# Optimization experiments

Measured on AMD Instinct MI355X. Metric: run time of the kernel, lower is better.

The kernel has to match this reference:

```python
import jax, jax.numpy as jnp
import numpy as np

HIDDEN = 1024
HEADS = 16
HEAD_DIM = HIDDEN // HEADS  # 64
LOCAL = (128, 128)
ROPE_MAX_POS = LOCAL[0] + LOCAL[1]  # 256 (local attention branch)
ROPE_BASE = 10000.0


def make_rope_cache(max_len, dim, base):
    positions = jnp.arange(max_len, dtype=jnp.float32)
    theta = 1.0 / base ** (jnp.arange(0, dim, 2, dtype=jnp.float32) / dim)
    angles = jnp.einsum('i,j->ij', positions, theta)
    return jnp.stack([jnp.cos(angles), jnp.sin(angles)], axis=-1)  # (max_len, dim//2, 2)


def apply_rope(x, cache):
    # x: (B, S, H, D); cache: (max_pos, D//2, 2)
    S = x.shape[1]
    pos = jnp.arange(S) % cache.shape[0]
    rc = cache[pos][None, :, None, :, :]  # (1, S, 1, D//2, 2)
    xr = x.reshape(*x.shape[:-1], -1, 2)
    x0, x1 = xr[..., 0], xr[..., 1]
    c, s = rc[..., 0], rc[..., 1]
    out = jnp.stack([x0 * c - x1 * s, x1 * c + x0 * s], axis=-1)
    return out.reshape(x.shape)


def sliding_window_mask(S, window, dtype):
    rel = jnp.arange(S)[:, None] - jnp.arange(S)[None, :]
    inside = (rel >= -window[0]) & (rel <= window[1])
    return jnp.where(inside, jnp.zeros((), dtype), -jnp.inf)[None, None]  # (1,1,S,S)


def setup_inputs() -> dict:
    key = jax.random.key(0)
    k1, k2, k3, k4, k5 = jax.random.split(key, 5)
    B, S = 2, 2048
    hidden_states = jax.random.normal(k1, (B, S, HIDDEN), dtype=jnp.float32)
    Wqkv_kernel = jax.random.normal(k2, (HIDDEN, 3 * HIDDEN), dtype=jnp.float32) / np.sqrt(HIDDEN)
    Wqkv_bias = jnp.zeros((3 * HIDDEN,), dtype=jnp.float32)
    Wo_kernel = jax.random.normal(k3, (HIDDEN, HIDDEN), dtype=jnp.float32) / np.sqrt(HIDDEN)
    Wo_bias = jnp.zeros((HIDDEN,), dtype=jnp.float32)
    rope_cache = make_rope_cache(ROPE_MAX_POS, HEAD_DIM, ROPE_BASE)
    return {
        'hidden_states': hidden_states,
        'Wqkv_kernel': Wqkv_kernel,
        'Wqkv_bias': Wqkv_bias,
        'Wo_kernel': Wo_kernel,
        'Wo_bias': Wo_bias,
        'rope_cache': rope_cache,
    }


def reference(hidden_states, Wqkv_kernel, Wqkv_bias, Wo_kernel, Wo_bias, rope_cache):
    B, S, _ = hidden_states.shape
    qkv = hidden_states @ Wqkv_kernel + Wqkv_bias  # (B,S,3*HIDDEN)
    qkv = qkv.reshape(B, S, 3, HEADS, HEAD_DIM)
    q = qkv[:, :, 0]  # (B,S,H,D)
    k = qkv[:, :, 1]
    v = qkv[:, :, 2]
    q = apply_rope(q, rope_cache)
    k = apply_rope(k, rope_cache)
    # to (B,H,S,D)
    q = jnp.transpose(q, (0, 2, 1, 3))
    k = jnp.transpose(k, (0, 2, 1, 3))
    v = jnp.transpose(v, (0, 2, 1, 3))
    scale = jnp.sqrt(jnp.float32(HEAD_DIM))
    scores = jnp.einsum('bhqd,bhkd->bhqk', q, k) / scale
    mask = sliding_window_mask(S, LOCAL, scores.dtype)
    probs = jax.nn.softmax(scores + mask, axis=-1)
    out = jnp.einsum('bhqk,bhkd->bqhd', probs, v).reshape(B, S, HIDDEN)
    out = out @ Wo_kernel + Wo_bias
    return out
```

## Files before the change

### kernel.cpp

```cpp
#include <hip/hip_runtime.h>
#include <hip/hip_bf16.h>

typedef __bf16 bf16x8 __attribute__((ext_vector_type(8)));
typedef __bf16 bf16x4 __attribute__((ext_vector_type(4)));
typedef float f32x4 __attribute__((ext_vector_type(4)));

#define SLEN 2048
#define NHEADS 16
#define HDIM 64

__global__ __launch_bounds__(256) void prep(const float* __restrict__ hidden,
                                            const float* __restrict__ Wqkv,
                                            const float* __restrict__ Wo,
                                            __bf16* __restrict__ A1,
                                            __bf16* __restrict__ Wt,
                                            __bf16* __restrict__ Wot) {
    int b = blockIdx.x;
    if (b < 4096) {
        int i = b * 256 + threadIdx.x;
        float4 v = reinterpret_cast<const float4*>(hidden)[i];
        bf16x4 o = { (__bf16)v.x, (__bf16)v.y, (__bf16)v.z, (__bf16)v.w };
        reinterpret_cast<bf16x4*>(A1)[i] = o;
    } else {
        __shared__ float tile[32][33];
        const float* W; __bf16* Dst; int N, bx, by;
        if (b < 7168) { int bb = b - 4096; W = Wqkv; Dst = Wt;  N = 3072; bx = bb % 96; by = bb / 96; }
        else          { int bb = b - 7168; W = Wo;   Dst = Wot; N = 1024; bx = bb % 32; by = bb / 32; }
        int tx = threadIdx.x & 31, ty = threadIdx.x >> 5;
        int n0 = bx * 32, k0 = by * 32;
        #pragma unroll
        for (int i = ty; i < 32; i += 8)
            tile[i][tx] = W[(size_t)(k0 + i) * N + n0 + tx];
        __syncthreads();
        #pragma unroll
        for (int i = ty; i < 32; i += 8)
            Dst[(size_t)(n0 + i) * 1024 + k0 + tx] = (__bf16)tile[tx][i];
    }
}

template <int TN>
__global__ __launch_bounds__(256) void gemm_bt(const __bf16* __restrict__ A,
                                               const __bf16* __restrict__ Bt,
                                               const float* __restrict__ bias,
                                               float* __restrict__ Cf,
                                               __bf16* __restrict__ Cq,
                                               __bf16* __restrict__ Ck,
                                               __bf16* __restrict__ Cv,
                                               int M, int N, int K, int epi) {
    constexpr int JN = TN / 32;
    __shared__ __align__(16) __bf16 As[128 * 40];
    __shared__ __align__(16) __bf16 Bs[TN * 40];

    int nb = N / TN;
    int bx = blockIdx.x % nb;
    int by = blockIdx.x / nb;
    int row0 = by * 128, col0 = bx * TN;

    int tid = threadIdx.x;
    int wave = tid >> 6, lane = tid & 63;
    int quad = lane >> 4, lrow = lane & 15;
    int wm = wave >> 1, wn = wave & 1;

    int r1 = tid >> 2;
    int kk = (tid & 3) * 8;
    const __bf16* Aptr = A + (size_t)(row0 + r1) * K + kk;
    const __bf16* Bptr = Bt + (size_t)(col0 + r1) * K + kk;

    f32x4 acc[4][JN];
    f32x4 zero = {0.f, 0.f, 0.f, 0.f};
    #pragma unroll
    for (int i = 0; i < 4; i++)
        #pragma unroll
        for (int j = 0; j < JN; j++) acc[i][j] = zero;

    for (int k0 = 0; k0 < K; k0 += 32) {
        bf16x8 a0 = *reinterpret_cast<const bf16x8*>(Aptr + k0);
        bf16x8 a1 = *reinterpret_cast<const bf16x8*>(Aptr + (size_t)64 * K + k0);
        bf16x8 b0 = *reinterpret_cast<const bf16x8*>(Bptr + k0);
        bf16x8 b1;
        if (TN == 128) b1 = *reinterpret_cast<const bf16x8*>(Bptr + (size_t)64 * K + k0);
        __syncthreads();
        *reinterpret_cast<bf16x8*>(&As[r1 * 40 + kk]) = a0;
        *reinterpret_cast<bf16x8*>(&As[(r1 + 64) * 40 + kk]) = a1;
        *reinterpret_cast<bf16x8*>(&Bs[r1 * 40 + kk]) = b0;
        if (TN == 128) *reinterpret_cast<bf16x8*>(&Bs[(r1 + 64) * 40 + kk]) = b1;
        __syncthreads();

        bf16x8 af[4], bfr[JN];
        #pragma unroll
        for (int i = 0; i < 4; i++)
            af[i] = *reinterpret_cast<const bf16x8*>(&As[(wm * 64 + i * 16 + lrow) * 40 + quad * 8]);
        #pragma unroll
        for (int j = 0; j < JN; j++)
            bfr[j] = *reinterpret_cast<const bf16x8*>(&Bs[(wn * (TN / 2) + j * 16 + lrow) * 40 + quad * 8]);
        #pragma unroll
        for (int i = 0; i < 4; i++)
            #pragma unroll
            for (int j = 0; j < JN; j++)
                acc[i][j] = __builtin_amdgcn_mfma_f32_16x16x32_bf16(af[i], bfr[j], acc[i][j], 0, 0, 0);
    }

    int part = col0 >> 10;
    #pragma unroll
    for (int i = 0; i < 4; i++) {
        int rowb = row0 + wm * 64 + i * 16 + quad * 4;
        #pragma unroll
        for (int j = 0; j < JN; j++) {
            int col = col0 + wn * (TN / 2) + j * 16 + lrow;
            float bsv = bias[col];
            #pragma unroll
            for (int r = 0; r < 4; r++) {
                int row = rowb + r;
                float v = acc[i][j][r] + bsv;
                if (epi == 0) {
                    Cf[(size_t)row * N + col] = v;
                } else {
                    int h = (col >> 6) & 15;
                    int d = col & 63;
                    int b = row >> 11;
                    int s = row & 2047;
                    __bf16* dst = (part == 0) ? Cq : ((part == 1) ? Ck : Cv);
                    dst[((size_t)(b * NHEADS + h) * SLEN + s) * HDIM + d] = (__bf16)v;
                }
            }
        }
    }
}

__device__ __forceinline__ bf16x8 rope8(bf16x8 v, f32x4 a, f32x4 b) {
    bf16x8 o;
    float e, od;
    e = (float)v[0]; od = (float)v[1];
    o[0] = (__bf16)(e * a[0] - od * a[1]); o[1] = (__bf16)(od * a[0] + e * a[1]);
    e = (float)v[2]; od = (float)v[3];
    o[2] = (__bf16)(e * a[2] - od * a[3]); o[3] = (__bf16)(od * a[2] + e * a[3]);
    e = (float)v[4]; od = (float)v[5];
    o[4] = (__bf16)(e * b[0] - od * b[1]); o[5] = (__bf16)(od * b[0] + e * b[1]);
    e = (float)v[6]; od = (float)v[7];
    o[6] = (__bf16)(e * b[2] - od * b[3]); o[7] = (__bf16)(od * b[2] + e * b[3]);
    return o;
}

__global__ __launch_bounds__(256) void attn_kernel(const __bf16* __restrict__ Q,
                                                   const __bf16* __restrict__ K,
                                                   const __bf16* __restrict__ V,
                                                   const float* __restrict__ rope,
                                                   __bf16* __restrict__ O) {
    __shared__ __align__(16) __bf16 Vt[64][328];
    __shared__ __align__(16) __bf16 Pl[4][16][40];

    int qt = blockIdx.x & 31;
    int bh = blockIdx.x >> 5;
    int q0 = qt * 64;
    int kbase0 = q0 - 128;
    const __bf16* Qbh = Q + (size_t)bh * SLEN * HDIM;
    const __bf16* Kbh = K + (size_t)bh * SLEN * HDIM;
    const __bf16* Vbh = V + (size_t)bh * SLEN * HDIM;

    int tid = threadIdx.x;
    int wave = tid >> 6, lane = tid & 63;
    int quad = lane >> 4, lrow = lane & 15;
    int wq0 = q0 + wave * 16;

    {
        int dchunk = wave * 16;
        #pragma unroll
        for (int k = 0; k < 5; k++) {
            int off = k * 64 + lane;
            int krow = kbase0 + off;
            krow = min(max(krow, 0), SLEN - 1);
            const __bf16* vp = Vbh + (size_t)krow * HDIM + dchunk;
            bf16x8 v0 = *reinterpret_cast<const bf16x8*>(vp);
            bf16x8 v1 = *reinterpret_cast<const bf16x8*>(vp + 8);
            #pragma unroll
            for (int i = 0; i < 8; i++) {
                Vt[dchunk + i][off] = v0[i];
                Vt[dchunk + 8 + i][off] = v1[i];
            }
        }
    }

    int posq = (wq0 + lrow) & 255;
    const float* rq = rope + (size_t)posq * 64;
    f32x4 qc0a = *reinterpret_cast<const f32x4*>(rq + quad * 8);
    f32x4 qc0b = *reinterpret_cast<const f32x4*>(rq + quad * 8 + 4);
    f32x4 qc1a = *reinterpret_cast<const f32x4*>(rq + 32 + quad * 8);
    f32x4 qc1b = *reinterpret_cast<const f32x4*>(rq + 32 + quad * 8 + 4);
    bf16x8 qb0 = rope8(*reinterpret_cast<const bf16x8*>(Qbh + (size_t)(wq0 + lrow) * HDIM + quad * 8),
                       qc0a, qc0b);
    bf16x8 qb1 = rope8(*reinterpret_cast<const bf16x8*>(Qbh + (size_t)(wq0 + lrow) * HDIM + 32 + quad * 8),
                       qc1a, qc1b);

    __syncthreads();

    f32x4 zero = {0.f, 0.f, 0.f, 0.f};
    f32x4 acc[4], acc_l = zero;
    #pragma unroll
    for (int t = 0; t < 4; t++) acc[t] = zero;

    bf16x8 ones = { (__bf16)1.f, (__bf16)1.f, (__bf16)1.f, (__bf16)1.f,
                    (__bf16)1.f, (__bf16)1.f, (__bf16)1.f, (__bf16)1.f };

    int cbeg = wave >> 1;
    if (q0 < 128) { int e = (128 - q0) >> 5; if (e > cbeg) cbeg = e; }
    int cend = (16 * wave + 271) >> 5;
    { int e = (2175 - q0) >> 5; if (e < cend) cend = e; }

    for (int c = cbeg; c <= cend; c++) {
        int kb = kbase0 + c * 32;
        int loc = c * 32;

        f32x4 st[2];
        #pragma unroll
        for (int sub = 0; sub < 2; sub++) {
            int kr = kb + sub * 16 + lrow;
            int krc = min(max(kr, 0), SLEN - 1);
            const __bf16* kp = Kbh + (size_t)krc * HDIM;
            const float* rk = rope + (size_t)(krc & 255) * 64;
            f32x4 kc0a = *reinterpret_cast<const f32x4*>(rk + quad * 8);
            f32x4 kc0b = *reinterpret_cast<const f32x4*>(rk + quad * 8 + 4);
            f32x4 kc1a = *reinterpret_cast<const f32x4*>(rk + 32 + quad * 8);
            f32x4 kc1b = *reinterpret_cast<const f32x4*>(rk + 32 + quad * 8 + 4);
            bf16x8 ka0 = rope8(*reinterpret_cast<const bf16x8*>(kp + quad * 8), kc0a, kc0b);
            bf16x8 ka1 = rope8(*reinterpret_cast<const bf16x8*>(kp + 32 + quad * 8), kc1a, kc1b);
            st[sub] = __builtin_amdgcn_mfma_f32_16x16x32_bf16(ka0, qb0, zero, 0, 0, 0);
            st[sub] = __builtin_amdgcn_mfma_f32_16x16x32_bf16(ka1, qb1, st[sub], 0, 0, 0);
        }

        int q = wq0 + lrow;
        #pragma unroll
        for (int sub = 0; sub < 2; sub++) {
            bf16x4 pk;
            #pragma unroll
            for (int r = 0; r < 4; r++) {
                int key = kb + sub * 16 + quad * 4 + r;
                int rel = key - q;
                bool valid = (rel >= -128) && (rel <= 128) && (key >= 0) && (key < SLEN);
                float p = valid ? __expf(st[sub][r] * 0.125f) : 0.0f;
                pk[r] = (__bf16)p;
            }
            *reinterpret_cast<bf16x4*>(&Pl[wave][lrow][sub * 16 + quad * 4]) = pk;
        }
        asm volatile("s_waitcnt lgkmcnt(0)" ::: "memory");

        bf16x8 bp = *reinterpret_cast<const bf16x8*>(&Pl[wave][lrow][quad * 8]);
        acc_l = __builtin_amdgcn_mfma_f32_16x16x32_bf16(ones, bp, acc_l, 0, 0, 0);
        #pragma unroll
        for (int t = 0; t < 4; t++) {
            bf16x8 va = *reinterpret_cast<const bf16x8*>(&Vt[t * 16 + lrow][loc + quad * 8]);
            acc[t] = __builtin_amdgcn_mfma_f32_16x16x32_bf16(va, bp, acc[t], 0, 0, 0);
        }
    }

    float inv = 1.0f / acc_l[0];
    int b = bh >> 4, h = bh & 15;
    int q = wq0 + lrow;
    size_t base = ((size_t)b * SLEN + q) * 1024 + h * HDIM;
    #pragma unroll
    for (int t = 0; t < 4; t++) {
        bf16x4 o;
        #pragma unroll
        for (int r = 0; r < 4; r++) o[r] = (__bf16)(acc[t][r] * inv);
        *reinterpret_cast<bf16x4*>(&O[base + t * 16 + quad * 4]) = o;
    }
}

extern "C" void kernel_launch(void* const* d_in, const int* in_sizes, int n_in,
                              void* d_out, int out_size, void* d_ws, size_t ws_size,
                              hipStream_t stream) {
    const float* hidden = (const float*)d_in[0];
    const float* Wqkv   = (const float*)d_in[1];
    const float* bqkv   = (const float*)d_in[2];
    const float* Wo     = (const float*)d_in[3];
    const float* bo     = (const float*)d_in[4];
    const float* rope   = (const float*)d_in[5];
    float* out = (float*)d_out;

    char* ws = (char*)d_ws;
    __bf16* A1  = (__bf16*)(ws);
    __bf16* Wt  = (__bf16*)(ws + 8388608);
    __bf16* Wot = (__bf16*)(ws + 14680064);
    __bf16* Qb  = (__bf16*)(ws + 16777216);
    __bf16* Kb  = (__bf16*)(ws + 25165824);
    __bf16* Vb  = (__bf16*)(ws + 33554432);
    __bf16* AO  = (__bf16*)(ws + 41943040);

    prep<<<8192, 256, 0, stream>>>(hidden, Wqkv, Wo, A1, Wt, Wot);

    gemm_bt<128><<<32 * 24, 256, 0, stream>>>(A1, Wt, bqkv, nullptr, Qb, Kb, Vb,
                                              4096, 3072, 1024, 1);
    attn_kernel<<<1024, 256, 0, stream>>>(Qb, Kb, Vb, rope, AO);
    gemm_bt<64><<<32 * 16, 256, 0, stream>>>(AO, Wot, bo, out, nullptr, nullptr, nullptr,
                                             4096, 1024, 1024, 0);
}
```

Before: 211.6 us.

## Move RoPE into separate in-place kernel and prefetch next K tile in attention

Applies rotary embedding to Q and K once in a standalone elementwise kernel instead of re-rotating each K row inside the attention loop, where every key row was rotated roughly ten times across overlapping windows. The attention loop now software-prefetches the next K chunk into registers while computing the current one. This adds an extra kernel launch and a full read-modify-write pass over Q and K with scalar bf16 accesses. It also raises register pressure from double-buffered K fragments.

```diff
diff --git a/kernel.cpp b/kernel.cpp
--- a/kernel.cpp
+++ b/kernel.cpp
@@ -127,24 +127,28 @@
     }
 }
 
-__device__ __forceinline__ bf16x8 rope8(bf16x8 v, f32x4 a, f32x4 b) {
-    bf16x8 o;
-    float e, od;
-    e = (float)v[0]; od = (float)v[1];
-    o[0] = (__bf16)(e * a[0] - od * a[1]); o[1] = (__bf16)(od * a[0] + e * a[1]);
-    e = (float)v[2]; od = (float)v[3];
-    o[2] = (__bf16)(e * a[2] - od * a[3]); o[3] = (__bf16)(od * a[2] + e * a[3]);
-    e = (float)v[4]; od = (float)v[5];
-    o[4] = (__bf16)(e * b[0] - od * b[1]); o[5] = (__bf16)(od * b[0] + e * b[1]);
-    e = (float)v[6]; od = (float)v[7];
-    o[6] = (__bf16)(e * b[2] - od * b[3]); o[7] = (__bf16)(od * b[2] + e * b[3]);
-    return o;
+__global__ __launch_bounds__(256) void rope_kernel(__bf16* __restrict__ Q,
+                                                   __bf16* __restrict__ K,
+                                                   const float* __restrict__ rope) {
+    int idx = blockIdx.x * 256 + threadIdx.x;
+    int p = idx & 31;
+    int s = (idx >> 5) & 2047;
+    int bh = idx >> 16;
+    size_t off = ((size_t)bh * SLEN + s) * HDIM + 2 * p;
+    int pos = s & 255;
+    float c = rope[(pos * 32 + p) * 2];
+    float sn = rope[(pos * 32 + p) * 2 + 1];
+    float q0 = (float)Q[off], q1 = (float)Q[off + 1];
+    Q[off]     = (__bf16)(q0 * c - q1 * sn);
+    Q[off + 1] = (__bf16)(q1 * c + q0 * sn);
+    float k0 = (float)K[off], k1 = (float)K[off + 1];
+    K[off]     = (__bf16)(k0 * c - k1 * sn);
+    K[off + 1] = (__bf16)(k1 * c + k0 * sn);
 }
 
 __global__ __launch_bounds__(256) void attn_kernel(const __bf16* __restrict__ Q,
                                                    const __bf16* __restrict__ K,
                                                    const __bf16* __restrict__ V,
-                                                   const float* __restrict__ rope,
                                                    __bf16* __restrict__ O) {
     __shared__ __align__(16) __bf16 Vt[64][328];
     __shared__ __align__(16) __bf16 Pl[4][16][40];
@@ -180,16 +184,8 @@
         }
     }
 
-    int posq = (wq0 + lrow) & 255;
-    const float* rq = rope + (size_t)posq * 64;
-    f32x4 qc0a = *reinterpret_cast<const f32x4*>(rq + quad * 8);
-    f32x4 qc0b = *reinterpret_cast<const f32x4*>(rq + quad * 8 + 4);
-    f32x4 qc1a = *reinterpret_cast<const f32x4*>(rq + 32 + quad * 8);
-    f32x4 qc1b = *reinterpret_cast<const f32x4*>(rq + 32 + quad * 8 + 4);
-    bf16x8 qb0 = rope8(*reinterpret_cast<const bf16x8*>(Qbh + (size_t)(wq0 + lrow) * HDIM + quad * 8),
-                       qc0a, qc0b);
-    bf16x8 qb1 = rope8(*reinterpret_cast<const bf16x8*>(Qbh + (size_t)(wq0 + lrow) * HDIM + 32 + quad * 8),
-                       qc1a, qc1b);
+    bf16x8 qb0 = *reinterpret_cast<const bf16x8*>(Qbh + (size_t)(wq0 + lrow) * HDIM + quad * 8);
+    bf16x8 qb1 = *reinterpret_cast<const bf16x8*>(Qbh + (size_t)(wq0 + lrow) * HDIM + 32 + quad * 8);
 
     __syncthreads();
 
@@ -206,25 +202,33 @@
     int cend = (16 * wave + 271) >> 5;
     { int e = (2175 - q0) >> 5; if (e < cend) cend = e; }
 
-    for (int c = cbeg; c <= cend; c++) {
+    auto loadK = [&](int c, bf16x8 kf[2][2]) {
         int kb = kbase0 + c * 32;
-        int loc = c * 32;
-
-        f32x4 st[2];
         #pragma unroll
         for (int sub = 0; sub < 2; sub++) {
             int kr = kb + sub * 16 + lrow;
             int krc = min(max(kr, 0), SLEN - 1);
             const __bf16* kp = Kbh + (size_t)krc * HDIM;
-            const float* rk = rope + (size_t)(krc & 255) * 64;
-            f32x4 kc0a = *reinterpret_cast<const f32x4*>(rk + quad * 8);
-            f32x4 kc0b = *reinterpret_cast<const f32x4*>(rk + quad * 8 + 4);
-            f32x4 kc1a = *reinterpret_cast<const f32x4*>(rk + 32 + quad * 8);
-            f32x4 kc1b = *reinterpret_cast<const f32x4*>(rk + 32 + quad * 8 + 4);
-            bf16x8 ka0 = rope8(*reinterpret_cast<const bf16x8*>(kp + quad * 8), kc0a, kc0b);
-            bf16x8 ka1 = rope8(*reinterpret_cast<const bf16x8*>(kp + 32 + quad * 8), kc1a, kc1b);
-            st[sub] = __builtin_amdgcn_mfma_f32_16x16x32_bf16(ka0, qb0, zero, 0, 0, 0);
-            st[sub] = __builtin_amdgcn_mfma_f32_16x16x32_bf16(ka1, qb1, st[sub], 0, 0, 0);
+            kf[sub][0] = *reinterpret_cast<const bf16x8*>(kp + quad * 8);
+            kf[sub][1] = *reinterpret_cast<const bf16x8*>(kp + 32 + quad * 8);
+        }
+    };
+
+    bf16x8 ka[2][2];
+    loadK(cbeg, ka);
+
+    for (int c = cbeg; c <= cend; c++) {
+        bf16x8 kn[2][2];
+        if (c < cend) loadK(c + 1, kn);
+
+        int kb = kbase0 + c * 32;
+        int loc = c * 32;
+
+        f32x4 st[2];
+        #pragma unroll
+        for (int sub = 0; sub < 2; sub++) {
+            st[sub] = __builtin_amdgcn_mfma_f32_16x16x32_bf16(ka[sub][0], qb0, zero, 0, 0, 0);
+            st[sub] = __builtin_amdgcn_mfma_f32_16x16x32_bf16(ka[sub][1], qb1, st[sub], 0, 0, 0);
         }
 
         int q = wq0 + lrow;
@@ -250,6 +254,12 @@
             bf16x8 va = *reinterpret_cast<const bf16x8*>(&Vt[t * 16 + lrow][loc + quad * 8]);
             acc[t] = __builtin_amdgcn_mfma_f32_16x16x32_bf16(va, bp, acc[t], 0, 0, 0);
         }
+
+        #pragma unroll
+        for (int sub = 0; sub < 2; sub++) {
+            ka[sub][0] = kn[sub][0];
+            ka[sub][1] = kn[sub][1];
+        }
     }
 
     float inv = 1.0f / acc_l[0];
@@ -289,7 +299,8 @@
 
     gemm_bt<128><<<32 * 24, 256, 0, stream>>>(A1, Wt, bqkv, nullptr, Qb, Kb, Vb,
                                               4096, 3072, 1024, 1);
-    attn_kernel<<<1024, 256, 0, stream>>>(Qb, Kb, Vb, rope, AO);
+    rope_kernel<<<8192, 256, 0, stream>>>(Qb, Kb, rope);
+    attn_kernel<<<1024, 256, 0, stream>>>(Qb, Kb, Vb, AO);
     gemm_bt<64><<<32 * 16, 256, 0, stream>>>(AO, Wot, bo, out, nullptr, nullptr, nullptr,
                                              4096, 1024, 1024, 0);
 }
```

Result: faster. 190.3 us (-10.0%).
